# Optimization experiments

Measured on AMD Instinct MI355X. Metric: run time of the kernel, lower is better.

The kernel has to match this reference:

```python
import jax, jax.numpy as jnp
import numpy as np


def setup_inputs() -> dict:
    key = jax.random.key(0)
    k1, k2 = jax.random.split(key)
    img_render_points = jax.random.normal(k1, (128, 128, 2), dtype=jnp.float32)
    ref_catheter_contour_point_cloud = jax.random.normal(k2, (16384, 2), dtype=jnp.float32)
    return {
        "img_render_points": img_render_points,
        "ref_catheter_contour_point_cloud": ref_catheter_contour_point_cloud,
    }


def reference(img_render_points, ref_catheter_contour_point_cloud):
    # Flatten to point cloud (N, 2)
    pc = img_render_points.reshape(-1, 2)
    ref = ref_catheter_contour_point_cloud  # (M, 2)
    # Pairwise Euclidean distances (N, M); torch.norm(..., dim=2) equivalent
    diff = pc[:, None, :] - ref[None, :, :]          # (N, M, 2)
    distances = jnp.sqrt(jnp.sum(diff * diff, axis=-1))  # (N, M)
    min_d1 = jnp.min(distances, axis=1)  # nearest ref point for each render point
    min_d2 = jnp.min(distances, axis=0)  # nearest render point for each ref point
    chamfer_loss = jnp.sum(min_d1) + jnp.sum(min_d2)
    return chamfer_loss
```

## Files before the change

kernel.cpp:

```cpp
#include <hip/hip_runtime.h>
#include <math.h>

#define NPTS  16384
#define BLK   256
#define Q     8
#define QB    (NPTS / (BLK * Q))
#define TCH   64
#define CHUNK (NPTS / TCH)
#define G     (CHUNK / 4)


__global__ __launch_bounds__(BLK, 4) void cc_min_kernel(
        const float2* __restrict__ pc,
        const float2* __restrict__ ref,
        float* __restrict__ ws,
        float* __restrict__ out) {
    __shared__ float s6[G * 12];

    int b   = blockIdx.x;
    int dir = b / (QB * TCH);
    int rem = b % (QB * TCH);
    int qb  = rem / TCH;
    int ch  = rem % TCH;

    if (b == 0 && threadIdx.x == 0) out[0] = 0.0f;

    const float2* __restrict__ qry = dir ? ref : pc;
    const float2* __restrict__ tgt = dir ? pc  : ref;

    if (threadIdx.x < G) {
        int g = threadIdx.x;
        const float4* t4 = (const float4*)tgt + (size_t)ch * (CHUNK / 2);
        float4 p01 = t4[2 * g];
        float4 p23 = t4[2 * g + 1];
        float4* dst = (float4*)&s6[12 * g];
        dst[0] = make_float4(-2.0f * p01.x, -2.0f * p01.y,
                             -2.0f * p01.z, -2.0f * p01.w);
        dst[1] = make_float4(-2.0f * p23.x, -2.0f * p23.y,
                             -2.0f * p23.z, -2.0f * p23.w);
        dst[2] = make_float4(fmaf(p01.x, p01.x, p01.y * p01.y),
                             fmaf(p01.z, p01.z, p01.w * p01.w),
                             fmaf(p23.x, p23.x, p23.y * p23.y),
                             fmaf(p23.z, p23.z, p23.w * p23.w));
    }

    float px[Q], py[Q], pn[Q], m[Q];
    int qbase = qb * (BLK * Q) + threadIdx.x;
#pragma unroll
    for (int j = 0; j < Q; ++j) {
        float2 p = qry[qbase + j * BLK];
        px[j] = p.x;
        py[j] = p.y;
        pn[j] = fmaf(p.x, p.x, p.y * p.y);
        m[j]  = INFINITY;
    }
    __syncthreads();

#pragma unroll 4
    for (int g = 0; g < G; ++g) {
        float4 A = *(const float4*)&s6[12 * g];
        float4 B = *(const float4*)&s6[12 * g + 4];
        float4 C = *(const float4*)&s6[12 * g + 8];
#pragma unroll
        for (int j = 0; j < Q; ++j) {
            float s0 = fmaf(px[j], A.x, fmaf(py[j], A.y, C.x));
            float s1 = fmaf(px[j], A.z, fmaf(py[j], A.w, C.y));
            float s2 = fmaf(px[j], B.x, fmaf(py[j], B.y, C.z));
            float s3 = fmaf(px[j], B.z, fmaf(py[j], B.w, C.w));
            m[j] = fminf(fminf(m[j], s0), s1);
            m[j] = fminf(fminf(m[j], s2), s3);
        }
    }

    float* wrow = ws + (size_t)ch * (2 * NPTS) + dir * NPTS + qbase;
#pragma unroll
    for (int j = 0; j < Q; ++j) {
        wrow[j * BLK] = fmaxf(m[j] + pn[j], 0.0f);
    }
}

#define FBLK 128
__global__ __launch_bounds__(FBLK) void cc_final_kernel(
        const float* __restrict__ ws, float* __restrict__ out) {
    int q = blockIdx.x * FBLK + threadIdx.x;

    float mm[16];
#pragma unroll
    for (int k = 0; k < 16; ++k)
        mm[k] = ws[(size_t)k * (2 * NPTS) + q];
#pragma unroll
    for (int ch = 16; ch < TCH; ch += 16) {
#pragma unroll
        for (int k = 0; k < 16; ++k)
            mm[k] = fminf(mm[k], ws[(size_t)(ch + k) * (2 * NPTS) + q]);
    }
#pragma unroll
    for (int s2 = 8; s2 > 0; s2 >>= 1)
#pragma unroll
        for (int k = 0; k < 8; ++k)
            if (k < s2) mm[k] = fminf(mm[k], mm[k + s2]);

    float s = sqrtf(mm[0]);

#pragma unroll
    for (int off = 32; off > 0; off >>= 1)
        s += __shfl_down(s, off, 64);

    if ((threadIdx.x & 63) == 0)
        atomicAdd(out, s);
}

extern "C" void kernel_launch(void* const* d_in, const int* in_sizes, int n_in,
                              void* d_out, int out_size, void* d_ws, size_t ws_size,
                              hipStream_t stream) {
    const float2* pc  = (const float2*)d_in[0];
    const float2* ref = (const float2*)d_in[1];
    float* out = (float*)d_out;
    float* ws  = (float*)d_ws;

    cc_min_kernel<<<2 * QB * TCH, BLK, 0, stream>>>(pc, ref, ws, out);
    cc_final_kernel<<<(2 * NPTS) / FBLK, FBLK, 0, stream>>>(ws, out);
}
```

Before: 93.02 us.

## Precompute target table in global memory and read it via scalar loads

Adds a pack kernel that builds the -2*target and squared-norm table once in workspace, replacing per-block shared-memory staging. The min kernel reads that table with a wave-uniform index, so the compiler can use scalar loads and SGPR operands instead of LDS reads, and the barrier goes away. This costs an extra kernel launch, and scalar-cache latency may stall the inner loop.

```diff
diff --git a/kernel.cpp b/kernel.cpp
--- a/kernel.cpp
+++ b/kernel.cpp
@@ -7,42 +7,49 @@
 #define QB    (NPTS / (BLK * Q))
 #define TCH   64
 #define CHUNK (NPTS / TCH)
-#define G     (CHUNK / 4)
+#define G4    (CHUNK / 4)
+#define NG    (NPTS / 4)
 
+#define PART_FLOATS (TCH * 2 * NPTS)
+
+
+__global__ __launch_bounds__(BLK) void cc_pack_kernel(
+        const float2* __restrict__ pc,
+        const float2* __restrict__ ref,
+        float* __restrict__ ws,
+        float* __restrict__ out) {
+    int idx = blockIdx.x * BLK + threadIdx.x;
+    if (idx == 0) out[0] = 0.0f;
+    int dir = idx / NG;
+    int g   = idx - dir * NG;
+    const float4* src = (const float4*)(dir ? pc : ref);
+    float4 p01 = src[2 * g];
+    float4 p23 = src[2 * g + 1];
+    float4* tb = (float4*)(ws + PART_FLOATS) + (size_t)idx * 3;
+    tb[0] = make_float4(-2.0f * p01.x, -2.0f * p01.y,
+                        -2.0f * p01.z, -2.0f * p01.w);
+    tb[1] = make_float4(-2.0f * p23.x, -2.0f * p23.y,
+                        -2.0f * p23.z, -2.0f * p23.w);
+    tb[2] = make_float4(fmaf(p01.x, p01.x, p01.y * p01.y),
+                        fmaf(p01.z, p01.z, p01.w * p01.w),
+                        fmaf(p23.x, p23.x, p23.y * p23.y),
+                        fmaf(p23.z, p23.z, p23.w * p23.w));
+}
 
 __global__ __launch_bounds__(BLK, 4) void cc_min_kernel(
         const float2* __restrict__ pc,
         const float2* __restrict__ ref,
-        float* __restrict__ ws,
-        float* __restrict__ out) {
-    __shared__ float s6[G * 12];
-
+        float* __restrict__ ws) {
     int b   = blockIdx.x;
     int dir = b / (QB * TCH);
     int rem = b % (QB * TCH);
     int qb  = rem / TCH;
     int ch  = rem % TCH;
 
-    if (b == 0 && threadIdx.x == 0) out[0] = 0.0f;
+    const float2* __restrict__ qry = dir ? ref : pc;
 
-    const float2* __restrict__ qry = dir ? ref : pc;
-    const float2* __restrict__ tgt = dir ? pc  : ref;
-
-    if (threadIdx.x < G) {
-        int g = threadIdx.x;
-        const float4* t4 = (const float4*)tgt + (size_t)ch * (CHUNK / 2);
-        float4 p01 = t4[2 * g];
-        float4 p23 = t4[2 * g + 1];
-        float4* dst = (float4*)&s6[12 * g];
-        dst[0] = make_float4(-2.0f * p01.x, -2.0f * p01.y,
-                             -2.0f * p01.z, -2.0f * p01.w);
-        dst[1] = make_float4(-2.0f * p23.x, -2.0f * p23.y,
-                             -2.0f * p23.z, -2.0f * p23.w);
-        dst[2] = make_float4(fmaf(p01.x, p01.x, p01.y * p01.y),
-                             fmaf(p01.z, p01.z, p01.w * p01.w),
-                             fmaf(p23.x, p23.x, p23.y * p23.y),
-                             fmaf(p23.z, p23.z, p23.w * p23.w));
-    }
+    int tbase = __builtin_amdgcn_readfirstlane(3 * (dir * NG + ch * G4));
+    const float4* __restrict__ tbl = (const float4*)(ws + PART_FLOATS);
 
     float px[Q], py[Q], pn[Q], m[Q];
     int qbase = qb * (BLK * Q) + threadIdx.x;
@@ -54,19 +61,19 @@
         pn[j] = fmaf(p.x, p.x, p.y * p.y);
         m[j]  = INFINITY;
     }
-    __syncthreads();
 
 #pragma unroll 4
-    for (int g = 0; g < G; ++g) {
-        float4 A = *(const float4*)&s6[12 * g];
-        float4 B = *(const float4*)&s6[12 * g + 4];
-        float4 C = *(const float4*)&s6[12 * g + 8];
+    for (int g = 0; g < G4; ++g) {
+        float4 A = tbl[tbase + 3 * g];
+        float4 B = tbl[tbase + 3 * g + 1];
+        float4 Z = tbl[tbase + 3 * g + 2];
+        float z0 = Z.x, z1 = Z.y, z2 = Z.z, z3 = Z.w;
 #pragma unroll
         for (int j = 0; j < Q; ++j) {
-            float s0 = fmaf(px[j], A.x, fmaf(py[j], A.y, C.x));
-            float s1 = fmaf(px[j], A.z, fmaf(py[j], A.w, C.y));
-            float s2 = fmaf(px[j], B.x, fmaf(py[j], B.y, C.z));
-            float s3 = fmaf(px[j], B.z, fmaf(py[j], B.w, C.w));
+            float s0 = fmaf(px[j], A.x, fmaf(py[j], A.y, z0));
+            float s1 = fmaf(px[j], A.z, fmaf(py[j], A.w, z1));
+            float s2 = fmaf(px[j], B.x, fmaf(py[j], B.y, z2));
+            float s3 = fmaf(px[j], B.z, fmaf(py[j], B.w, z3));
             m[j] = fminf(fminf(m[j], s0), s1);
             m[j] = fminf(fminf(m[j], s2), s3);
         }
@@ -118,6 +125,7 @@
     float* out = (float*)d_out;
     float* ws  = (float*)d_ws;
 
-    cc_min_kernel<<<2 * QB * TCH, BLK, 0, stream>>>(pc, ref, ws, out);
+    cc_pack_kernel<<<(2 * NG) / BLK, BLK, 0, stream>>>(pc, ref, ws, out);
+    cc_min_kernel<<<2 * QB * TCH, BLK, 0, stream>>>(pc, ref, ws);
     cc_final_kernel<<<(2 * NPTS) / FBLK, FBLK, 0, stream>>>(ws, out);
 }
```

After: 104.2 us. 12.1% more time.
